# Optimization experiments

Measured on AMD Instinct MI355X. Metric: run time of the kernel, lower is better.

The kernel has to match this reference:

```python
import jax, jax.numpy as jnp
import numpy as np

B, N, D = 16384, 30, 128  # batch, max_neighbors, model_dim


def setup_inputs() -> dict:
    key = jax.random.key(0)
    k1, k2, k3, k4, k5 = jax.random.split(key, 5)
    rel_embeds = jax.random.normal(k1, (B, N, D), dtype=jnp.float32)
    ent_embeds = jax.random.normal(k2, (B, N, D), dtype=jnp.float32)
    mask = jax.random.randint(k3, (B, N), 0, 2).astype(jnp.bool_)  # True = masked
    # neigh_att_W: Linear(2D -> D), xavier-normal weight; neigh_att_u: Linear(D -> 1)
    std_w = float(np.sqrt(2.0 / (2 * D + D)))
    W_w = jax.random.normal(k4, (D, 2 * D), dtype=jnp.float32) * std_w
    b_w = jnp.zeros((D,), dtype=jnp.float32)
    std_u = float(np.sqrt(2.0 / (D + 1)))
    W_u = jax.random.normal(k5, (1, D), dtype=jnp.float32) * std_u
    b_u = jnp.zeros((1,), dtype=jnp.float32)
    return {"rel_embeds": rel_embeds, "ent_embeds": ent_embeds, "mask": mask,
            "W_w": W_w, "b_w": b_w, "W_u": W_u, "b_u": b_u}


def reference(rel_embeds, ent_embeds, mask, W_w, b_w, W_u, b_u):
    # concat along feature dim -> [B, N, 2D]
    concat = jnp.concatenate([rel_embeds, ent_embeds], axis=-1)
    h = jnp.tanh(jnp.einsum('bnf,df->bnd', concat, W_w) + b_w)      # [B, N, D]
    att = jnp.einsum('bnd,od->bno', h, W_u) + b_u                   # [B, N, 1]
    att = jnp.where(mask[..., None], -jnp.inf, att)
    att = jax.nn.softmax(att, axis=1)[..., 0]                       # [B, N]
    out = jnp.einsum('bn,bnd->bd', att, ent_embeds)                 # [B, D]
    return jnp.tanh(out)
```

## Files before the change

### kernel.cpp

```cpp
#include <hip/hip_runtime.h>
#include <cstdint>
#include <cstddef>


#define WAVES 4
#define BLOCK 256
#define ROWS 64
#define LDS_STRIDE 264

typedef __attribute__((ext_vector_type(8))) short short8;
typedef __attribute__((ext_vector_type(4))) float f32x4;

__device__ __forceinline__ float fast_tanh(float x) {
  float e = __expf(2.0f * x);
  return 1.0f - 2.0f / (e + 1.0f);
}

__device__ __forceinline__ void cvt_hilo(float f, unsigned int& h, unsigned int& l) {
  unsigned int bits = __float_as_uint(f);
  h = bits >> 16;
  float r = f - __uint_as_float(bits & 0xFFFF0000u);
  l = __float_as_uint(r) >> 16;
}

template <int CTRL>
__device__ __forceinline__ float dpp_add(float x) {
  return x + __int_as_float(
      __builtin_amdgcn_update_dpp(0, __float_as_int(x), CTRL, 0xF, 0xF, true));
}
__device__ __forceinline__ float row16_sum(float x) {
  x = dpp_add<0xB1>(x);
  x = dpp_add<0x4E>(x);
  x = dpp_add<0x141>(x);
  x = dpp_add<0x140>(x);
  return x;
}

__global__ __launch_bounds__(BLOCK, 2) void hetrognn_kernel(
    const float* __restrict__ rel, const float* __restrict__ ent,
    const int* __restrict__ mask, const float* __restrict__ Ww,
    const float* __restrict__ bw, const float* __restrict__ Wu,
    const float* __restrict__ bu, float* __restrict__ out, int Btot) {
  __shared__ unsigned short Ahi[ROWS * LDS_STRIDE];
  __shared__ unsigned short Alo[ROWS * LDS_STRIDE];
  __shared__ float pscore[WAVES][ROWS];
  __shared__ float att[ROWS];

  const int tid = threadIdx.x;
  const int wave = tid >> 6;
  const int lane = tid & 63;
  const int l15 = lane & 15;
  const int quad = lane >> 4;

  short8 whi[2][8], wlo[2][8];
  float bwv[2], uv[2];
#pragma unroll
  for (int c = 0; c < 2; ++c) {
    const int d = wave * 32 + c * 16 + l15;
    bwv[c] = bw[d];
    uv[c] = Wu[d];
#pragma unroll
    for (int ks = 0; ks < 8; ++ks) {
      const float* wp = Ww + d * 256 + ks * 32 + quad * 8;
#pragma unroll
      for (int j = 0; j < 8; ++j) {
        unsigned int h, l;
        cvt_hilo(wp[j], h, l);
        whi[c][ks][j] = (short)h;
        wlo[c][ks][j] = (short)l;
      }
    }
  }
  const float buv = bu[0];

  const int pairs = (Btot + 1) >> 1;
  for (int p = blockIdx.x; p < pairs; p += gridDim.x) {
    const int bA = p * 2;
    const int bB = bA + 1;

    int mreg = 1;
    if (tid < 64) {
      const int n = tid & 31;
      const int bb = bA + (tid >> 5);
      if (n < 30 && bb < Btot) mreg = mask[(size_t)bb * 30 + n];
    }

#pragma unroll
    for (int half = 0; half < 2; ++half) {
      const int bb = bA + half;
      const bool bvalid = (bb < Btot);
      const float* rb = rel + (size_t)bb * 3840;
      const float* eb = ent + (size_t)bb * 3840;
      const int rowbase = half * 32;
#pragma unroll
      for (int it = 0; it < 8; ++it) {
        const int i4 = tid + it * 256;
        const int row = i4 >> 6;
        const int k4 = (i4 & 63) << 2;
        float4 v = make_float4(0.f, 0.f, 0.f, 0.f);
        if (bvalid && row < 30) {
          const float* src = (k4 < 128) ? (rb + row * 128 + k4)
                                        : (eb + row * 128 + (k4 - 128));
          v = *(const float4*)src;
        }
        unsigned int h0, h1, h2, h3, l0, l1, l2, l3;
        cvt_hilo(v.x, h0, l0);
        cvt_hilo(v.y, h1, l1);
        cvt_hilo(v.z, h2, l2);
        cvt_hilo(v.w, h3, l3);
        uint2 hh, ll;
        hh.x = h0 | (h1 << 16);
        hh.y = h2 | (h3 << 16);
        ll.x = l0 | (l1 << 16);
        ll.y = l2 | (l3 << 16);
        *(uint2*)&Ahi[(rowbase + row) * LDS_STRIDE + k4] = hh;
        *(uint2*)&Alo[(rowbase + row) * LDS_STRIDE + k4] = ll;
      }
      asm volatile("" ::: "memory");
    }
    __syncthreads();

#pragma unroll
    for (int mt = 0; mt < 4; ++mt) {
      f32x4 acc0 = {0.f, 0.f, 0.f, 0.f};
      f32x4 acc1 = {0.f, 0.f, 0.f, 0.f};
      const int arow = mt * 16 + l15;
      const unsigned short* abase = &Ahi[arow * LDS_STRIDE + quad * 8];
      const unsigned short* lbase = &Alo[arow * LDS_STRIDE + quad * 8];
#pragma unroll
      for (int ks = 0; ks < 8; ++ks) {
        short8 ah = *(const short8*)(abase + ks * 32);
        short8 al = *(const short8*)(lbase + ks * 32);
        acc0 = __builtin_amdgcn_mfma_f32_16x16x32_bf16(ah, whi[0][ks], acc0, 0, 0, 0);
        acc1 = __builtin_amdgcn_mfma_f32_16x16x32_bf16(ah, whi[1][ks], acc1, 0, 0, 0);
        acc0 = __builtin_amdgcn_mfma_f32_16x16x32_bf16(al, whi[0][ks], acc0, 0, 0, 0);
        acc1 = __builtin_amdgcn_mfma_f32_16x16x32_bf16(al, whi[1][ks], acc1, 0, 0, 0);
        acc0 = __builtin_amdgcn_mfma_f32_16x16x32_bf16(ah, wlo[0][ks], acc0, 0, 0, 0);
        acc1 = __builtin_amdgcn_mfma_f32_16x16x32_bf16(ah, wlo[1][ks], acc1, 0, 0, 0);
      }
      float part[4];
#pragma unroll
      for (int reg = 0; reg < 4; ++reg) {
        float h0 = fast_tanh(acc0[reg] + bwv[0]);
        float h1 = fast_tanh(acc1[reg] + bwv[1]);
        part[reg] = uv[0] * h0 + uv[1] * h1;
      }
#pragma unroll
      for (int reg = 0; reg < 4; ++reg) part[reg] = row16_sum(part[reg]);
      float pv = (l15 == 0) ? part[0] : (l15 == 1) ? part[1] : (l15 == 2) ? part[2] : part[3];
      if (l15 < 4) pscore[wave][mt * 16 + quad * 4 + l15] = pv;
    }
    __syncthreads();

    if (tid < 64) {
      const int n = tid & 31;
      const int base = tid & 32;
      float raw = pscore[0][base + n] + pscore[1][base + n] +
                  pscore[2][base + n] + pscore[3][base + n] + buv;
      const bool valid = (n < 30) && (mreg == 0);
      float sc = valid ? raw : -INFINITY;
      float mx = sc;
#pragma unroll
      for (int m = 1; m < 32; m <<= 1) mx = fmaxf(mx, __shfl_xor(mx, m, 32));
      float e = valid ? __expf(sc - mx) : 0.f;
      float sm = e;
#pragma unroll
      for (int m = 1; m < 32; m <<= 1) sm += __shfl_xor(sm, m, 32);
      att[base + n] = e / sm;
    }
    __syncthreads();

    {
      const int half = tid >> 7;
      const int d = tid & 127;
      const int bb = bA + half;
      if (bb < Btot) {
        const float* ep = ent + (size_t)bb * 3840 + d;
        const float* ap = &att[half * 32];
        float a0 = 0.f, a1 = 0.f;
#pragma unroll
        for (int n = 0; n < 30; n += 2) {
          a0 += ap[n] * ep[n * 128];
          a1 += ap[n + 1] * ep[(n + 1) * 128];
        }
        out[(size_t)bb * 128 + d] = fast_tanh(a0 + a1);
      }
    }
    __syncthreads();
  }
}

extern "C" void kernel_launch(void* const* d_in, const int* in_sizes, int n_in,
                              void* d_out, int out_size, void* d_ws, size_t ws_size,
                              hipStream_t stream) {
  const float* rel = (const float*)d_in[0];
  const float* ent = (const float*)d_in[1];
  const int* mask = (const int*)d_in[2];
  const float* Ww = (const float*)d_in[3];
  const float* bw = (const float*)d_in[4];
  const float* Wu = (const float*)d_in[5];
  const float* bu = (const float*)d_in[6];
  float* out = (float*)d_out;
  const int Btot = in_sizes[0] / 3840;
  const int grid = 2048;
  hipLaunchKernelGGL(hetrognn_kernel, dim3(grid), dim3(BLOCK), 0, stream,
                     rel, ent, mask, Ww, bw, Wu, bu, out, Btot);
}
```

Measured before the change: 649.5 us.

## Split output columns across eight waves per block instead of four

Doubles the block to 512 threads so each wave owns 16 output columns instead of 32. This halves the per-wave weight registers and MFMA chain, and raises waves per block for latency hiding while staging work is split across more threads. In exchange every wave re-reads the same A tiles from LDS, the score reduction sums eight partials, half the block idles in the final weighted-sum stage, and barriers now span more waves.

```diff
diff --git a/kernel.cpp b/kernel.cpp
--- a/kernel.cpp
+++ b/kernel.cpp
@@ -3,8 +3,8 @@
 #include <cstddef>
 
 
-#define WAVES 4
-#define BLOCK 256
+#define WAVES 8
+#define BLOCK 512
 #define ROWS 64
 #define LDS_STRIDE 264
 
@@ -36,7 +36,7 @@
   return x;
 }
 
-__global__ __launch_bounds__(BLOCK, 2) void hetrognn_kernel(
+__global__ __launch_bounds__(BLOCK, 4) void hetrognn_kernel(
     const float* __restrict__ rel, const float* __restrict__ ent,
     const int* __restrict__ mask, const float* __restrict__ Ww,
     const float* __restrict__ bw, const float* __restrict__ Wu,
@@ -52,23 +52,19 @@
   const int l15 = lane & 15;
   const int quad = lane >> 4;
 
-  short8 whi[2][8], wlo[2][8];
-  float bwv[2], uv[2];
+  short8 whi[8], wlo[8];
+  const int d = wave * 16 + l15;
+  const float bwv = bw[d];
+  const float uv = Wu[d];
 #pragma unroll
-  for (int c = 0; c < 2; ++c) {
-    const int d = wave * 32 + c * 16 + l15;
-    bwv[c] = bw[d];
-    uv[c] = Wu[d];
+  for (int ks = 0; ks < 8; ++ks) {
+    const float* wp = Ww + d * 256 + ks * 32 + quad * 8;
 #pragma unroll
-    for (int ks = 0; ks < 8; ++ks) {
-      const float* wp = Ww + d * 256 + ks * 32 + quad * 8;
-#pragma unroll
-      for (int j = 0; j < 8; ++j) {
-        unsigned int h, l;
-        cvt_hilo(wp[j], h, l);
-        whi[c][ks][j] = (short)h;
-        wlo[c][ks][j] = (short)l;
-      }
+    for (int j = 0; j < 8; ++j) {
+      unsigned int h, l;
+      cvt_hilo(wp[j], h, l);
+      whi[ks][j] = (short)h;
+      wlo[ks][j] = (short)l;
     }
   }
   const float buv = bu[0];
@@ -76,7 +72,6 @@
   const int pairs = (Btot + 1) >> 1;
   for (int p = blockIdx.x; p < pairs; p += gridDim.x) {
     const int bA = p * 2;
-    const int bB = bA + 1;
 
     int mreg = 1;
     if (tid < 64) {
@@ -93,8 +88,8 @@
       const float* eb = ent + (size_t)bb * 3840;
       const int rowbase = half * 32;
 #pragma unroll
-      for (int it = 0; it < 8; ++it) {
-        const int i4 = tid + it * 256;
+      for (int it = 0; it < 4; ++it) {
+        const int i4 = tid + it * 512;
         const int row = i4 >> 6;
         const int k4 = (i4 & 63) << 2;
         float4 v = make_float4(0.f, 0.f, 0.f, 0.f);
@@ -122,8 +117,7 @@
 
 #pragma unroll
     for (int mt = 0; mt < 4; ++mt) {
-      f32x4 acc0 = {0.f, 0.f, 0.f, 0.f};
-      f32x4 acc1 = {0.f, 0.f, 0.f, 0.f};
+      f32x4 acc = {0.f, 0.f, 0.f, 0.f};
       const int arow = mt * 16 + l15;
       const unsigned short* abase = &Ahi[arow * LDS_STRIDE + quad * 8];
       const unsigned short* lbase = &Alo[arow * LDS_STRIDE + quad * 8];
@@ -131,20 +125,13 @@
       for (int ks = 0; ks < 8; ++ks) {
         short8 ah = *(const short8*)(abase + ks * 32);
         short8 al = *(const short8*)(lbase + ks * 32);
-        acc0 = __builtin_amdgcn_mfma_f32_16x16x32_bf16(ah, whi[0][ks], acc0, 0, 0, 0);
-        acc1 = __builtin_amdgcn_mfma_f32_16x16x32_bf16(ah, whi[1][ks], acc1, 0, 0, 0);
-        acc0 = __builtin_amdgcn_mfma_f32_16x16x32_bf16(al, whi[0][ks], acc0, 0, 0, 0);
-        acc1 = __builtin_amdgcn_mfma_f32_16x16x32_bf16(al, whi[1][ks], acc1, 0, 0, 0);
-        acc0 = __builtin_amdgcn_mfma_f32_16x16x32_bf16(ah, wlo[0][ks], acc0, 0, 0, 0);
-        acc1 = __builtin_amdgcn_mfma_f32_16x16x32_bf16(ah, wlo[1][ks], acc1, 0, 0, 0);
+        acc = __builtin_amdgcn_mfma_f32_16x16x32_bf16(ah, whi[ks], acc, 0, 0, 0);
+        acc = __builtin_amdgcn_mfma_f32_16x16x32_bf16(al, whi[ks], acc, 0, 0, 0);
+        acc = __builtin_amdgcn_mfma_f32_16x16x32_bf16(ah, wlo[ks], acc, 0, 0, 0);
       }
       float part[4];
 #pragma unroll
-      for (int reg = 0; reg < 4; ++reg) {
-        float h0 = fast_tanh(acc0[reg] + bwv[0]);
-        float h1 = fast_tanh(acc1[reg] + bwv[1]);
-        part[reg] = uv[0] * h0 + uv[1] * h1;
-      }
+      for (int reg = 0; reg < 4; ++reg) part[reg] = uv * fast_tanh(acc[reg] + bwv);
 #pragma unroll
       for (int reg = 0; reg < 4; ++reg) part[reg] = row16_sum(part[reg]);
       float pv = (l15 == 0) ? part[0] : (l15 == 1) ? part[1] : (l15 == 2) ? part[2] : part[3];
@@ -155,8 +142,9 @@
     if (tid < 64) {
       const int n = tid & 31;
       const int base = tid & 32;
-      float raw = pscore[0][base + n] + pscore[1][base + n] +
-                  pscore[2][base + n] + pscore[3][base + n] + buv;
+      float raw = buv;
+#pragma unroll
+      for (int w = 0; w < WAVES; ++w) raw += pscore[w][base + n];
       const bool valid = (n < 30) && (mreg == 0);
       float sc = valid ? raw : -INFINITY;
       float mx = sc;
@@ -170,12 +158,12 @@
     }
     __syncthreads();
 
-    {
+    if (tid < 256) {
       const int half = tid >> 7;
-      const int d = tid & 127;
+      const int dd = tid & 127;
       const int bb = bA + half;
       if (bb < Btot) {
-        const float* ep = ent + (size_t)bb * 3840 + d;
+        const float* ep = ent + (size_t)bb * 3840 + dd;
         const float* ap = &att[half * 32];
         float a0 = 0.f, a1 = 0.f;
 #pragma unroll
@@ -183,7 +171,7 @@
           a0 += ap[n] * ep[n * 128];
           a1 += ap[n + 1] * ep[(n + 1) * 128];
         }
-        out[(size_t)bb * 128 + d] = fast_tanh(a0 + a1);
+        out[(size_t)bb * 128 + dd] = fast_tanh(a0 + a1);
       }
     }
     __syncthreads();
```

New measurement: 600.4 us. 7.6% less time.
